# Kernel tuning notes

Measured on AMD Instinct MI355X. Metric: run time of the kernel, lower is better.

The kernel has to match this reference:

```python
import jax, jax.numpy as jnp
import numpy as np

HIDDEN = 2048
NUM_HEADS = 6
HEAD_V = 512          # head_dim * expand_v = 256 * 2
VALUE_DIM = NUM_HEADS * HEAD_V  # 3072
CONV_K = 4
PHASE_BASE = 10000.0
EPS = 1e-5


def _causal_depthwise_conv(x, w):
    # x: [B, T, C], w: [C, K]; causal depthwise conv, no bias, no activation
    B, T, C = x.shape
    K = w.shape[1]
    xp = jnp.pad(x, ((0, 0), (K - 1, 0), (0, 0)))
    y = jnp.zeros_like(x)
    for j in range(K):
        y = y + xp[:, j:j + T, :] * w[:, j]
    return y


def _rotate(x, ang):
    # x: [..., D] interleaved RoPE pairs, ang: [..., D//2] pair angles
    cos = jnp.cos(ang)
    sin = jnp.sin(ang)
    xe = x[..., ::2]
    xo = x[..., 1::2]
    ye = xe * cos - xo * sin
    yo = xo * cos + xe * sin
    return jnp.stack([ye, yo], axis=-1).reshape(x.shape)


def setup_inputs() -> dict:
    key = jax.random.key(0)
    ks = jax.random.split(key, 12)
    s = 0.02
    return {
        "hidden_states": jax.random.normal(ks[0], (2, 2048, HIDDEN), jnp.float32),
        "Wq": jax.random.normal(ks[1], (HIDDEN, VALUE_DIM), jnp.float32) * s,
        "Wk": jax.random.normal(ks[2], (HIDDEN, VALUE_DIM), jnp.float32) * s,
        "Wv": jax.random.normal(ks[3], (HIDDEN, VALUE_DIM), jnp.float32) * s,
        "Wa": jax.random.normal(ks[4], (HIDDEN, NUM_HEADS), jnp.float32) * s,
        "Wb": jax.random.normal(ks[5], (HIDDEN, NUM_HEADS), jnp.float32) * s,
        "Wg": jax.random.normal(ks[6], (HIDDEN, VALUE_DIM), jnp.float32) * s,
        "Wo": jax.random.normal(ks[7], (VALUE_DIM, HIDDEN), jnp.float32) * s,
        "conv_q": jax.random.normal(ks[8], (VALUE_DIM, CONV_K), jnp.float32) * s,
        "conv_k": jax.random.normal(ks[9], (VALUE_DIM, CONV_K), jnp.float32) * s,
        "conv_v": jax.random.normal(ks[10], (VALUE_DIM, CONV_K), jnp.float32) * s,
        "rms_w": jnp.ones((HEAD_V,), jnp.float32),
    }


def _forward(hidden_states, Wq, Wk, Wv, Wa, Wb, Wg, Wo, conv_q, conv_k, conv_v, rms_w):
    B, T, _ = hidden_states.shape
    H, D = NUM_HEADS, HEAD_V
    inv_freq = 1.0 / (PHASE_BASE ** (jnp.arange(0, D, 2, dtype=jnp.float32) / D))  # [D/2]

    q = _causal_depthwise_conv(hidden_states @ Wq, conv_q).reshape(B, T, H, D)
    k = _causal_depthwise_conv(hidden_states @ Wk, conv_k).reshape(B, T, H, D)
    v = _causal_depthwise_conv(hidden_states @ Wv, conv_v).reshape(B, T, H, D)

    # pair angles (RoPE-style): raw even channels scaled by inverse frequencies
    theta = q[..., ::2] * inv_freq           # [B, T, H, D/2] output/query phase
    psi = k[..., ::2] * inv_freq             # write phase
    # state rotation per step = phase increment so cumulative state phase tracks theta
    phi = theta - jnp.concatenate([jnp.zeros_like(theta[:, :1]), theta[:, :-1]], axis=1)

    alpha = jax.nn.sigmoid(hidden_states @ Wa)  # [B, T, H] decay gate
    beta = jax.nn.sigmoid(hidden_states @ Wb)   # [B, T, H] write gate

    # time-major scan inputs
    tm = lambda a: jnp.moveaxis(a, 1, 0)
    xs = (tm(theta), tm(psi), tm(phi), tm(v), tm(alpha), tm(beta))

    def step(state, inp):
        th, ps, ph, vt, at, bt = inp  # state: [B, H, D]
        retained = _rotate(state, ph) * at[..., None]
        write = _rotate(vt, ps)
        new_state = retained + bt[..., None] * write
        out_t = _rotate(new_state, -th)
        return new_state, out_t

    state0 = jnp.zeros((B, H, D), hidden_states.dtype)
    _, out = jax.lax.scan(step, state0, xs)     # out: [T, B, H, D]
    out = jnp.moveaxis(out, 0, 1)               # [B, T, H, D]

    # gated RMSNorm over head_v_dim, then output projection
    g = (hidden_states @ Wg).reshape(B, T, H, D)
    rms = jax.lax.rsqrt(jnp.mean(jnp.square(out), axis=-1, keepdims=True) + EPS)
    o = out * rms * rms_w * jax.nn.silu(g)
    return (o.reshape(B, T, VALUE_DIM) @ Wo)


def reference(hidden_states, Wq, Wk, Wv, Wa, Wb, Wg, Wo, conv_q, conv_k, conv_v, rms_w):
    return _forward(hidden_states, Wq, Wk, Wv, Wa, Wb, Wg, Wo, conv_q, conv_k, conv_v, rms_w)
```

## Files before the change

### kernel.cpp

```cpp
#include <hip/hip_runtime.h>
#include <hip/hip_bf16.h>
#include <stdint.h>

using bf16 = __hip_bfloat16;
using mfrag = __attribute__((ext_vector_type(8))) __bf16;
using f32x4 = __attribute__((ext_vector_type(4))) float;

#define TOKENS 4096
#define HID    2048
#define VD     3072
#define NH     6
#define HD     512
#define NPAIR  256
#define N1     9216
#define NC     64
#define CHUNK  32

__device__ __forceinline__ void gld_lds16(const bf16* g, bf16* l) {
    __builtin_amdgcn_global_load_lds((const __attribute__((address_space(1))) void*)g,
                                     (__attribute__((address_space(3))) void*)l, 16, 0, 0);
}

template<int BN_T>
__global__ __launch_bounds__(512, 2) void k_gemm2(const bf16* __restrict__ A,
                                                  const bf16* __restrict__ Bt,
                                                  void* __restrict__ Cv,
                                                  int M, int N, int K, int obf) {
    constexpr int WN   = (BN_T == 256) ? 4 : 2;
    constexpr int WM   = 8 / WN;
    constexpr int MF   = (256 / WM) / 16;
    constexpr int NHT  = 2 + BN_T / 128;
    constexpr int HT   = 16384;
    constexpr int SLOT = NHT * HT;

    extern __shared__ char smem[];
    const int tid  = threadIdx.x;
    const int wave = tid >> 6;
    const int lane = tid & 63;
    const int lrow = lane & 15;
    const int lk   = lane >> 4;
    const int wm   = wave / WN;
    const int wn   = wave % WN;

    const int nbn = N / BN_T;
    const int bid = blockIdx.x;
    const int xcd = bid & 7;
    const int k   = bid >> 3;
    const int rn  = nbn >> 1;
    const int j   = k & 31;
    const int bm  = ((((xcd >> 1) << 2) + (j & 3)) << 8);
    const int bn  = ((xcd & 1) * rn + (k >> 5) * 8 + (j >> 2)) * BN_T;

    const int NT = K >> 6;

    auto stage_ht = [&](const bf16* src, int row0, char* htb, int koff) {
#pragma unroll
        for (int i = 0; i < 2; ++i) {
            const int L = i * 512 + tid;
            const int r = L >> 3;
            const int c = (L & 7) ^ (r & 7);
            gld_lds16(src + (size_t)(row0 + r) * K + koff + c * 8,
                      (bf16*)(htb + (size_t)L * 16));
        }
    };
    auto STAGE = [&](int t, char* sb) {
        const int ko = t << 6;
        stage_ht(A, bm,       sb,          ko);
        stage_ht(A, bm + 128, sb + HT,     ko);
        stage_ht(Bt, bn,      sb + 2 * HT, ko);
        if (BN_T == 256) stage_ht(Bt, bn + 128, sb + 3 * HT, ko);
    };

    auto rdA = [&](const char* rb, int mf, int kk) -> mfrag {
        const int r  = wm * (MF * 16) + mf * 16 + lrow;
        const int ht = r >> 7, lr = r & 127;
        const int cc = (kk * 4 + lk) ^ (lr & 7);
        return *(const mfrag*)(rb + (size_t)ht * HT + (size_t)lr * 128 + cc * 16);
    };
    auto rdB = [&](const char* rb, int nf, int kk) -> mfrag {
        const int r  = wn * 64 + nf * 16 + lrow;
        const int ht = r >> 7, lr = r & 127;
        const int cc = (kk * 4 + lk) ^ (lr & 7);
        return *(const mfrag*)(rb + (size_t)(2 + ht) * HT + (size_t)lr * 128 + cc * 16);
    };

    f32x4 acc[MF][4];
#pragma unroll
    for (int m = 0; m < MF; ++m)
#pragma unroll
        for (int n = 0; n < 4; ++n) acc[m][n] = f32x4{0.f, 0.f, 0.f, 0.f};

    STAGE(0, smem);
    asm volatile("s_waitcnt vmcnt(0)" ::: "memory");
    __builtin_amdgcn_sched_barrier(0);
    __builtin_amdgcn_s_barrier();

    for (int kt = 0; kt < NT; ++kt) {
        char* rb = smem + (size_t)(kt & 1) * SLOT;
        char* wb = smem + (size_t)((kt + 1) & 1) * SLOT;
        if (kt + 1 < NT) STAGE(kt + 1, wb);

        mfrag bfr[4][2];
#pragma unroll
        for (int nf = 0; nf < 4; ++nf)
#pragma unroll
            for (int kk = 0; kk < 2; ++kk) bfr[nf][kk] = rdB(rb, nf, kk);

#pragma unroll
        for (int h2 = 0; h2 < 2; ++h2) {
            mfrag af[MF / 2][2];
#pragma unroll
            for (int mf = 0; mf < MF / 2; ++mf)
#pragma unroll
                for (int kk = 0; kk < 2; ++kk) af[mf][kk] = rdA(rb, h2 * (MF / 2) + mf, kk);
            __builtin_amdgcn_s_setprio(1);
#pragma unroll
            for (int mf = 0; mf < MF / 2; ++mf)
#pragma unroll
                for (int nf = 0; nf < 4; ++nf) {
                    const int mi = h2 * (MF / 2) + mf;
                    acc[mi][nf] = __builtin_amdgcn_mfma_f32_16x16x32_bf16(af[mf][0], bfr[nf][0], acc[mi][nf], 0, 0, 0);
                    acc[mi][nf] = __builtin_amdgcn_mfma_f32_16x16x32_bf16(af[mf][1], bfr[nf][1], acc[mi][nf], 0, 0, 0);
                }
            __builtin_amdgcn_s_setprio(0);
        }

        if (kt + 1 < NT) {
            asm volatile("s_waitcnt vmcnt(0)" ::: "memory");
            __builtin_amdgcn_sched_barrier(0);
            __builtin_amdgcn_s_barrier();
            __builtin_amdgcn_sched_barrier(0);
        }
    }

#pragma unroll
    for (int m = 0; m < MF; ++m)
#pragma unroll
        for (int j2 = 0; j2 < 4; ++j2) {
            const int r = bm + wm * (MF * 16) + m * 16 + lk * 4 + j2;
#pragma unroll
            for (int n = 0; n < 4; ++n) {
                const int c = bn + wn * 64 + n * 16 + lrow;
                if (obf) ((bf16*)Cv)[(size_t)r * N + c] = __float2bfloat16(acc[m][n][j2]);
                else     ((float*)Cv)[(size_t)r * N + c] = acc[m][n][j2];
            }
        }
}

__global__ void k_prep_w(const float* __restrict__ Wq, const float* __restrict__ Wk,
                         const float* __restrict__ Wv, const float* __restrict__ Wg,
                         bf16* __restrict__ Wt) {
    __shared__ float t[32][33];
    const int n0 = blockIdx.x * 32;
    const int k0 = blockIdx.y * 32;
    const int tx = threadIdx.x, ty = threadIdx.y;
    const float* src; int cb, cs;
    if (n0 < 1536)      { int m = n0;        src = Wq; cb = (m >> 8) * 512 + (m & 255) * 2; cs = 2; }
    else if (n0 < 3072) { int m = n0 - 1536; src = Wk; cb = (m >> 8) * 512 + (m & 255) * 2; cs = 2; }
    else if (n0 < 6144) { int m = n0 - 3072; src = Wv; cb = m; cs = 1; }
    else                { int m = n0 - 6144; src = Wg; cb = m; cs = 1; }
#pragma unroll
    for (int i = 0; i < 4; ++i) {
        int k = k0 + ty + i * 8;
        t[ty + i * 8][tx] = src[(size_t)k * VD + cb + cs * tx];
    }
    __syncthreads();
#pragma unroll
    for (int i = 0; i < 4; ++i) {
        int n = n0 + ty + i * 8;
        Wt[(size_t)n * HID + k0 + tx] = __float2bfloat16(t[tx][ty + i * 8]);
    }
}

__global__ void k_tr_cast(const float* __restrict__ src, bf16* __restrict__ dst, int R, int Ccol) {
    __shared__ float t[32][33];
    const int c0 = blockIdx.x * 32, r0 = blockIdx.y * 32;
    const int tx = threadIdx.x, ty = threadIdx.y;
#pragma unroll
    for (int i = 0; i < 4; ++i)
        t[ty + i * 8][tx] = src[(size_t)(r0 + ty + i * 8) * Ccol + c0 + tx];
    __syncthreads();
#pragma unroll
    for (int i = 0; i < 4; ++i)
        dst[(size_t)(c0 + ty + i * 8) * R + r0 + tx] = __float2bfloat16(t[tx][ty + i * 8]);
}

__global__ __launch_bounds__(256) void k_ab(const float* __restrict__ hs, const float* __restrict__ Wa,
                                            const float* __restrict__ Wb,
                                            float* __restrict__ alpha, float* __restrict__ beta,
                                            bf16* __restrict__ hsb) {
    const int tok = blockIdx.x;
    const int tid = threadIdx.x;
    float part[12];
#pragma unroll
    for (int j = 0; j < 12; ++j) part[j] = 0.f;
    const float* hrow = hs + (size_t)tok * HID;
    bf16* hbrow = hsb + (size_t)tok * HID;
    for (int i = 0; i < 8; ++i) {
        int k = i * 256 + tid;
        float x = hrow[k];
        hbrow[k] = __float2bfloat16(x);
        const float* wa = Wa + k * NH;
        const float* wb = Wb + k * NH;
#pragma unroll
        for (int j = 0; j < NH; ++j) {
            part[j]     = fmaf(x, wa[j], part[j]);
            part[6 + j] = fmaf(x, wb[j], part[6 + j]);
        }
    }
    __shared__ float red[12][4];
    const int lane = tid & 63, wv = tid >> 6;
#pragma unroll
    for (int j = 0; j < 12; ++j) {
        float s = part[j];
        for (int off = 32; off; off >>= 1) s += __shfl_down(s, off);
        if (lane == 0) red[j][wv] = s;
    }
    __syncthreads();
    if (tid < 12) {
        float s = red[tid][0] + red[tid][1] + red[tid][2] + red[tid][3];
        float v = 1.f / (1.f + expf(-s));
        if (tid < 6) alpha[(size_t)tok * NH + tid] = v;
        else         beta [(size_t)tok * NH + tid - 6] = v;
    }
}

__global__ __launch_bounds__(256) void k_scan1(const bf16* __restrict__ X,
                                               const float* __restrict__ alpha,
                                               const float* __restrict__ beta,
                                               const float* __restrict__ cq,
                                               const float* __restrict__ ck,
                                               const float* __restrict__ cv,
                                               float* __restrict__ U, float* __restrict__ pp) {
    const int bx = blockIdx.x;
    const int c  = bx % NC;
    const int h  = (bx / NC) % NH;
    const int b  = bx / (NC * NH);
    const int p  = threadIdx.x;
    const int t0 = c * CHUNK;
    const int ch2 = h * HD + 2 * p;
    const float wq0 = cq[ch2 * 4 + 0], wq1 = cq[ch2 * 4 + 1], wq2 = cq[ch2 * 4 + 2], wq3 = cq[ch2 * 4 + 3];
    const float wk0 = ck[ch2 * 4 + 0], wk1 = ck[ch2 * 4 + 1], wk2 = ck[ch2 * 4 + 2], wk3 = ck[ch2 * 4 + 3];
    const float wa0 = cv[ch2 * 4 + 0], wa1 = cv[ch2 * 4 + 1], wa2 = cv[ch2 * 4 + 2], wa3 = cv[ch2 * 4 + 3];
    const float wb0 = cv[(ch2 + 1) * 4 + 0], wb1 = cv[(ch2 + 1) * 4 + 1],
                wb2 = cv[(ch2 + 1) * 4 + 2], wb3 = cv[(ch2 + 1) * 4 + 3];
    const float invf = exp2f(-13.287712379549449f * ((float)p * (1.0f / 256.0f)));
    const int qcol = h * NPAIR + p;
    const int kcol = 1536 + h * NPAIR + p;
    const int vcol = 3072 + ch2;

    float xq[3], xk[3], xv0[3], xv1[3];
#pragma unroll
    for (int i = 0; i < 3; ++i) {
        int t = t0 - 3 + i;
        if (t >= 0) {
            size_t tok = (size_t)b * 2048 + t;
            const bf16* xr = X + tok * N1;
            xq[i] = __bfloat162float(xr[qcol]);
            xk[i] = __bfloat162float(xr[kcol]);
            __hip_bfloat162 vv = *(const __hip_bfloat162*)&xr[vcol];
            xv0[i] = __bfloat162float(vv.x);
            xv1[i] = __bfloat162float(vv.y);
        } else { xq[i] = xk[i] = xv0[i] = xv1[i] = 0.f; }
    }

    float u0 = 0.f, u1 = 0.f, ap = 1.f;
    for (int t = t0; t < t0 + CHUNK; ++t) {
        const size_t tok = (size_t)b * 2048 + t;
        const bf16* xr = X + tok * N1;
        float nq = __bfloat162float(xr[qcol]);
        float nk = __bfloat162float(xr[kcol]);
        __hip_bfloat162 vv = *(const __hip_bfloat162*)&xr[vcol];
        float nv0 = __bfloat162float(vv.x);
        float nv1 = __bfloat162float(vv.y);
        float yq  = wq3 * nq  + wq2 * xq[2]  + wq1 * xq[1]  + wq0 * xq[0];
        float yk  = wk3 * nk  + wk2 * xk[2]  + wk1 * xk[1]  + wk0 * xk[0];
        float yv0 = wa3 * nv0 + wa2 * xv0[2] + wa1 * xv0[1] + wa0 * xv0[0];
        float yv1 = wb3 * nv1 + wb2 * xv1[2] + wb1 * xv1[1] + wb0 * xv1[0];
        xq[0] = xq[1]; xq[1] = xq[2]; xq[2] = nq;
        xk[0] = xk[1]; xk[1] = xk[2]; xk[2] = nk;
        xv0[0] = xv0[1]; xv0[1] = xv0[2]; xv0[2] = nv0;
        xv1[0] = xv1[1]; xv1[1] = xv1[2]; xv1[2] = nv1;
        float theta = yq * invf, psi = yk * invf;
        float d = psi - theta, sn, cs;
        __sincosf(d, &sn, &cs);
        float w0 = yv0 * cs - yv1 * sn;
        float w1 = yv1 * cs + yv0 * sn;
        float a  = alpha[tok * NH + h];
        float bb = beta [tok * NH + h];
        u0 = fmaf(a, u0, bb * w0);
        u1 = fmaf(a, u1, bb * w1);
        ap *= a;
        *(float2*)&U[tok * (size_t)VD + h * HD + 2 * p] = float2{u0, u1};
        if (p == 0) pp[tok * NH + h] = ap;
    }
}

__global__ __launch_bounds__(512) void k_carry(const float* __restrict__ U, const float* __restrict__ pp,
                                               float* __restrict__ carry) {
    const int bh = blockIdx.x;
    const int b = bh / NH, h = bh % NH;
    const int d = threadIdx.x;
    float ue[NC], pv[NC];
#pragma unroll
    for (int c = 0; c < NC; ++c) {
        size_t tok = (size_t)b * 2048 + c * CHUNK + CHUNK - 1;
        ue[c] = U[tok * (size_t)VD + h * HD + d];
        pv[c] = pp[tok * NH + h];
    }
    float s = 0.f;
#pragma unroll
    for (int c = 0; c < NC; ++c) {
        carry[((size_t)bh * NC + c) * HD + d] = s;
        s = ue[c] + pv[c] * s;
    }
}

__global__ __launch_bounds__(256) void k_pass3(const float* __restrict__ U, const float* __restrict__ pp,
                                               const float* __restrict__ carry, const bf16* __restrict__ X,
                                               const float* __restrict__ rms_w, bf16* __restrict__ O) {
    const int bx = blockIdx.x;
    const int h = bx % NH;
    const size_t tok = bx / NH;
    const int b = (int)(tok >> 11);
    const int t = (int)(tok & 2047);
    const int c = t / CHUNK;
    const int tid = threadIdx.x;
    const int d = tid * 2;
    float2 uu = *(const float2*)&U[tok * (size_t)VD + h * HD + d];
    float  P  = pp[tok * NH + h];
    float2 cy = *(const float2*)&carry[((size_t)(b * NH + h) * NC + c) * HD + d];
    float u0 = fmaf(P, cy.x, uu.x);
    float u1 = fmaf(P, cy.y, uu.y);
    float s = u0 * u0 + u1 * u1;
    for (int off = 32; off; off >>= 1) s += __shfl_down(s, off);
    __shared__ float r4[4];
    const int lane = tid & 63, wv = tid >> 6;
    if (lane == 0) r4[wv] = s;
    __syncthreads();
    float tot = r4[0] + r4[1] + r4[2] + r4[3];
    float rms = rsqrtf(tot * (1.f / 512.f) + 1e-5f);
    __hip_bfloat162 gg = *(const __hip_bfloat162*)&X[tok * N1 + 6144 + h * HD + d];
    float g0 = __bfloat162float(gg.x), g1 = __bfloat162float(gg.y);
    float si0 = g0 / (1.f + expf(-g0));
    float si1 = g1 / (1.f + expf(-g1));
    float o0 = u0 * rms * rms_w[d]     * si0;
    float o1 = u1 * rms * rms_w[d + 1] * si1;
    __hip_bfloat162 ob;
    ob.x = __float2bfloat16(o0);
    ob.y = __float2bfloat16(o1);
    *(__hip_bfloat162*)&O[tok * (size_t)VD + h * HD + d] = ob;
}

extern "C" void kernel_launch(void* const* d_in, const int* in_sizes, int n_in,
                              void* d_out, int out_size, void* d_ws, size_t ws_size,
                              hipStream_t stream) {
    const float* hs   = (const float*)d_in[0];
    const float* Wq   = (const float*)d_in[1];
    const float* Wk   = (const float*)d_in[2];
    const float* Wv   = (const float*)d_in[3];
    const float* Wa   = (const float*)d_in[4];
    const float* Wb   = (const float*)d_in[5];
    const float* Wg   = (const float*)d_in[6];
    const float* Wo   = (const float*)d_in[7];
    const float* cq   = (const float*)d_in[8];
    const float* ck   = (const float*)d_in[9];
    const float* cv   = (const float*)d_in[10];
    const float* rmsw = (const float*)d_in[11];

    char* ws = (char*)d_ws;
    size_t off = 0;
    auto alloc = [&](size_t bytes) -> void* {
        void* p = ws + off;
        off = (off + bytes + 255) & ~(size_t)255;
        return p;
    };
    bf16*  hsb   = (bf16*) alloc((size_t)TOKENS * HID * 2);
    bf16*  Wt    = (bf16*) alloc((size_t)N1 * HID * 2);
    bf16*  Wot   = (bf16*) alloc((size_t)HID * VD * 2);
    bf16*  X     = (bf16*) alloc((size_t)TOKENS * N1 * 2);
    float* U     = (float*)alloc((size_t)TOKENS * VD * 4);
    float* alp   = (float*)alloc((size_t)TOKENS * NH * 4);
    float* bet   = (float*)alloc((size_t)TOKENS * NH * 4);
    float* pp    = (float*)alloc((size_t)TOKENS * NH * 4);
    float* carry = (float*)alloc((size_t)2 * NH * NC * HD * 4);
    bf16*  O     = (bf16*)Wt;

    hipFuncSetAttribute((const void*)k_gemm2<256>,
                        hipFuncAttributeMaxDynamicSharedMemorySize, 2 * 4 * 16384);
    hipFuncSetAttribute((const void*)k_gemm2<128>,
                        hipFuncAttributeMaxDynamicSharedMemorySize, 2 * 3 * 16384);

    k_prep_w<<<dim3(N1 / 32, HID / 32), dim3(32, 8), 0, stream>>>(Wq, Wk, Wv, Wg, Wt);
    k_tr_cast<<<dim3(HID / 32, VD / 32), dim3(32, 8), 0, stream>>>(Wo, Wot, VD, HID);
    k_ab<<<TOKENS, 256, 0, stream>>>(hs, Wa, Wb, alp, bet, hsb);
    k_gemm2<256><<<dim3((TOKENS / 256) * (N1 / 256)), 512, 2 * 4 * 16384, stream>>>(hsb, Wt, X, TOKENS, N1, HID, 1);
    k_scan1<<<2 * NH * NC, 256, 0, stream>>>(X, alp, bet, cq, ck, cv, U, pp);
    k_carry<<<2 * NH, 512, 0, stream>>>(U, pp, carry);
    k_pass3<<<TOKENS * NH, 256, 0, stream>>>(U, pp, carry, X, rmsw, O);
    k_gemm2<128><<<dim3((TOKENS / 256) * (HID / 128)), 512, 2 * 3 * 16384, stream>>>(O, Wot, d_out, TOKENS, HID, VD, 0);
}
```

Baseline: 353.3 us.

## Interleave per-half-tile LDS prefetch with MFMA quarters in GEMM main loop

Restructures the GEMM K-loop into four quarter-phases, each reading a slice of A fragments and issuing one half-tile global-to-LDS stage for the next (or next-next) K step. Prefetch of the B tile runs two steps ahead, and partial vmcnt waits replace the full drain. The aim is to spread memory issue across the compute and hide load latency better. In exchange it adds a barrier per quarter and tighter buffer reuse, which risks sync overhead or races on the double buffer.

```diff
diff --git a/kernel.cpp b/kernel.cpp
--- a/kernel.cpp
+++ b/kernel.cpp
@@ -22,13 +22,14 @@
 }
 
 template<int BN_T>
-__global__ __launch_bounds__(512, 2) void k_gemm2(const bf16* __restrict__ A,
+__global__ __launch_bounds__(512, 2) void k_gemm3(const bf16* __restrict__ A,
                                                   const bf16* __restrict__ Bt,
                                                   void* __restrict__ Cv,
                                                   int M, int N, int K, int obf) {
     constexpr int WN   = (BN_T == 256) ? 4 : 2;
     constexpr int WM   = 8 / WN;
     constexpr int MF   = (256 / WM) / 16;
+    constexpr int AQ   = MF / 4;
     constexpr int NHT  = 2 + BN_T / 128;
     constexpr int HT   = 16384;
     constexpr int SLOT = NHT * HT;
@@ -63,12 +64,14 @@
                       (bf16*)(htb + (size_t)L * 16));
         }
     };
-    auto STAGE = [&](int t, char* sb) {
+    auto ST = [&](int which, int t) {
+        if (t >= NT) return;
+        char* sb = smem + (size_t)(t & 1) * SLOT;
         const int ko = t << 6;
-        stage_ht(A, bm,       sb,          ko);
-        stage_ht(A, bm + 128, sb + HT,     ko);
-        stage_ht(Bt, bn,      sb + 2 * HT, ko);
-        if (BN_T == 256) stage_ht(Bt, bn + 128, sb + 3 * HT, ko);
+        if      (which == 0) stage_ht(A,  bm,       sb + 0 * HT, ko);
+        else if (which == 1) stage_ht(A,  bm + 128, sb + 1 * HT, ko);
+        else if (which == 2) stage_ht(Bt, bn,       sb + 2 * HT, ko);
+        else                 stage_ht(Bt, bn + 128, sb + 3 * HT, ko);
     };
 
     auto rdA = [&](const char* rb, int mf, int kk) -> mfrag {
@@ -90,46 +93,62 @@
 #pragma unroll
         for (int n = 0; n < 4; ++n) acc[m][n] = f32x4{0.f, 0.f, 0.f, 0.f};
 
-    STAGE(0, smem);
-    asm volatile("s_waitcnt vmcnt(0)" ::: "memory");
+    ST(2, 0);
+    if (BN_T == 256) ST(3, 0);
+    ST(0, 0);
+    ST(1, 0);
+    ST(2, 1);
+    asm volatile("s_waitcnt vmcnt(2)" ::: "memory");
     __builtin_amdgcn_sched_barrier(0);
     __builtin_amdgcn_s_barrier();
 
     for (int kt = 0; kt < NT; ++kt) {
-        char* rb = smem + (size_t)(kt & 1) * SLOT;
-        char* wb = smem + (size_t)((kt + 1) & 1) * SLOT;
-        if (kt + 1 < NT) STAGE(kt + 1, wb);
-
+        const char* rb = smem + (size_t)(kt & 1) * SLOT;
         mfrag bfr[4][2];
 #pragma unroll
-        for (int nf = 0; nf < 4; ++nf)
-#pragma unroll
-            for (int kk = 0; kk < 2; ++kk) bfr[nf][kk] = rdB(rb, nf, kk);
-
-#pragma unroll
-        for (int h2 = 0; h2 < 2; ++h2) {
-            mfrag af[MF / 2][2];
-#pragma unroll
-            for (int mf = 0; mf < MF / 2; ++mf)
-#pragma unroll
-                for (int kk = 0; kk < 2; ++kk) af[mf][kk] = rdA(rb, h2 * (MF / 2) + mf, kk);
+        for (int q = 0; q < 4; ++q) {
+            if (q == 0) {
+#pragma unroll
+                for (int nf = 0; nf < 4; ++nf)
+#pragma unroll
+                    for (int kk = 0; kk < 2; ++kk) bfr[nf][kk] = rdB(rb, nf, kk);
+            }
+            mfrag af[AQ][2];
+#pragma unroll
+            for (int i = 0; i < AQ; ++i)
+#pragma unroll
+                for (int kk = 0; kk < 2; ++kk) af[i][kk] = rdA(rb, q * AQ + i, kk);
+
+            if (BN_T == 256) {
+                if      (q == 0) ST(3, kt + 1);
+                else if (q == 1) ST(0, kt + 1);
+                else if (q == 2) ST(1, kt + 1);
+                else             ST(2, kt + 2);
+            } else {
+                if      (q == 0) ST(0, kt + 1);
+                else if (q == 1) ST(1, kt + 1);
+                else if (q == 2) ST(2, kt + 2);
+            }
+            if (q == 3 && kt + 1 < NT) {
+                if (kt + 2 < NT) { asm volatile("s_waitcnt vmcnt(2)" ::: "memory"); }
+                else             { asm volatile("s_waitcnt vmcnt(0)" ::: "memory"); }
+            }
+            __builtin_amdgcn_sched_barrier(0);
+            __builtin_amdgcn_s_barrier();
+            asm volatile("s_waitcnt lgkmcnt(0)" ::: "memory");
+            __builtin_amdgcn_sched_barrier(0);
             __builtin_amdgcn_s_setprio(1);
 #pragma unroll
-            for (int mf = 0; mf < MF / 2; ++mf)
+            for (int i = 0; i < AQ; ++i)
 #pragma unroll
                 for (int nf = 0; nf < 4; ++nf) {
-                    const int mi = h2 * (MF / 2) + mf;
-                    acc[mi][nf] = __builtin_amdgcn_mfma_f32_16x16x32_bf16(af[mf][0], bfr[nf][0], acc[mi][nf], 0, 0, 0);
-                    acc[mi][nf] = __builtin_amdgcn_mfma_f32_16x16x32_bf16(af[mf][1], bfr[nf][1], acc[mi][nf], 0, 0, 0);
+                    const int mi = q * AQ + i;
+                    acc[mi][nf] = __builtin_amdgcn_mfma_f32_16x16x32_bf16(af[i][0], bfr[nf][0], acc[mi][nf], 0, 0, 0);
+                    acc[mi][nf] = __builtin_amdgcn_mfma_f32_16x16x32_bf16(af[i][1], bfr[nf][1], acc[mi][nf], 0, 0, 0);
                 }
             __builtin_amdgcn_s_setprio(0);
-        }
-
-        if (kt + 1 < NT) {
-            asm volatile("s_waitcnt vmcnt(0)" ::: "memory");
             __builtin_amdgcn_sched_barrier(0);
             __builtin_amdgcn_s_barrier();
-            __builtin_amdgcn_sched_barrier(0);
         }
     }
 
@@ -386,17 +405,17 @@
     float* carry = (float*)alloc((size_t)2 * NH * NC * HD * 4);
     bf16*  O     = (bf16*)Wt;
 
-    hipFuncSetAttribute((const void*)k_gemm2<256>,
+    hipFuncSetAttribute((const void*)k_gemm3<256>,
                         hipFuncAttributeMaxDynamicSharedMemorySize, 2 * 4 * 16384);
-    hipFuncSetAttribute((const void*)k_gemm2<128>,
+    hipFuncSetAttribute((const void*)k_gemm3<128>,
                         hipFuncAttributeMaxDynamicSharedMemorySize, 2 * 3 * 16384);
 
     k_prep_w<<<dim3(N1 / 32, HID / 32), dim3(32, 8), 0, stream>>>(Wq, Wk, Wv, Wg, Wt);
     k_tr_cast<<<dim3(HID / 32, VD / 32), dim3(32, 8), 0, stream>>>(Wo, Wot, VD, HID);
     k_ab<<<TOKENS, 256, 0, stream>>>(hs, Wa, Wb, alp, bet, hsb);
-    k_gemm2<256><<<dim3((TOKENS / 256) * (N1 / 256)), 512, 2 * 4 * 16384, stream>>>(hsb, Wt, X, TOKENS, N1, HID, 1);
+    k_gemm3<256><<<dim3((TOKENS / 256) * (N1 / 256)), 512, 2 * 4 * 16384, stream>>>(hsb, Wt, X, TOKENS, N1, HID, 1);
     k_scan1<<<2 * NH * NC, 256, 0, stream>>>(X, alp, bet, cq, ck, cv, U, pp);
     k_carry<<<2 * NH, 512, 0, stream>>>(U, pp, carry);
     k_pass3<<<TOKENS * NH, 256, 0, stream>>>(U, pp, carry, X, rmsw, O);
-    k_gemm2<128><<<dim3((TOKENS / 256) * (HID / 128)), 512, 2 * 3 * 16384, stream>>>(O, Wot, d_out, TOKENS, HID, VD, 0);
-}
+    k_gemm3<128><<<dim3((TOKENS / 256) * (HID / 128)), 512, 2 * 3 * 16384, stream>>>(O, Wot, d_out, TOKENS, HID, VD, 0);
+}
```

New measurement: 369.8 us. +4.7%, slower.

## Split GEMM k-tile staging into four phases interleaved with MFMA quarters

Applied to the files above, without the earlier changes.

The GEMM main loop now splits each k-tile's compute into four MFMA phases. The next tile's global-to-LDS loads are issued in pieces (B halves and A row units) between those phases, and each phase is gated by a partial vmcnt wait plus a barrier instead of one full drain per tile. A-tile staging is reorganised so each unit loads exactly the rows a given MFMA quarter consumes. The goal is to overlap memory traffic with matrix math and avoid the stall at the end of every tile, at the cost of more barriers per iteration and fragile hand-tuned wait counts.

```diff
diff --git a/kernel.cpp b/kernel.cpp
--- a/kernel.cpp
+++ b/kernel.cpp
@@ -21,14 +21,20 @@
                                      (__attribute__((address_space(3))) void*)l, 16, 0, 0);
 }
 
+#define VMWAIT(n) asm volatile("s_waitcnt vmcnt(" #n ")" ::: "memory")
+#define SCHED0    __builtin_amdgcn_sched_barrier(0)
+#define SBAR      __builtin_amdgcn_s_barrier()
+
 template<int BN_T>
-__global__ __launch_bounds__(512, 2) void k_gemm2(const bf16* __restrict__ A,
+__global__ __launch_bounds__(512, 2) void k_gemm4(const bf16* __restrict__ A,
                                                   const bf16* __restrict__ Bt,
                                                   void* __restrict__ Cv,
                                                   int M, int N, int K, int obf) {
     constexpr int WN   = (BN_T == 256) ? 4 : 2;
     constexpr int WM   = 8 / WN;
     constexpr int MF   = (256 / WM) / 16;
+    constexpr int AQ   = MF / 4;
+    constexpr int SH   = AQ * 16;
     constexpr int NHT  = 2 + BN_T / 128;
     constexpr int HT   = 16384;
     constexpr int SLOT = NHT * HT;
@@ -45,30 +51,38 @@
     const int nbn = N / BN_T;
     const int bid = blockIdx.x;
     const int xcd = bid & 7;
-    const int k   = bid >> 3;
+    const int kk2 = bid >> 3;
     const int rn  = nbn >> 1;
-    const int j   = k & 31;
-    const int bm  = ((((xcd >> 1) << 2) + (j & 3)) << 8);
-    const int bn  = ((xcd & 1) * rn + (k >> 5) * 8 + (j >> 2)) * BN_T;
+    const int jj  = kk2 & 31;
+    const int bm  = ((((xcd >> 1) << 2) + (jj & 3)) << 8);
+    const int bn  = ((xcd & 1) * rn + (kk2 >> 5) * 8 + (jj >> 2)) * BN_T;
 
     const int NT = K >> 6;
 
-    auto stage_ht = [&](const bf16* src, int row0, char* htb, int koff) {
+    auto ST_B = [&](int half, int t) {
+        char* sb = smem + (size_t)(t & 1) * SLOT + (2 + half) * HT;
+        const int ko = t << 6;
 #pragma unroll
         for (int i = 0; i < 2; ++i) {
             const int L = i * 512 + tid;
             const int r = L >> 3;
             const int c = (L & 7) ^ (r & 7);
-            gld_lds16(src + (size_t)(row0 + r) * K + koff + c * 8,
-                      (bf16*)(htb + (size_t)L * 16));
+            gld_lds16(Bt + (size_t)(bn + half * 128 + r) * K + ko + c * 8,
+                      (bf16*)(sb + (size_t)L * 16));
         }
     };
-    auto STAGE = [&](int t, char* sb) {
+    auto ST_A = [&](int unit, int t) {
+        char* sb = smem + (size_t)(t & 1) * SLOT;
         const int ko = t << 6;
-        stage_ht(A, bm,       sb,          ko);
-        stage_ht(A, bm + 128, sb + HT,     ko);
-        stage_ht(Bt, bn,      sb + 2 * HT, ko);
-        if (BN_T == 256) stage_ht(Bt, bn + 128, sb + 3 * HT, ko);
+        const int s  = tid / (SH * 8);
+        const int W  = tid % (SH * 8);
+        const int rl = W >> 3;
+        const int c  = W & 7;
+        const int r256 = s * (256 / WM) + unit * SH + rl;
+        const int cl = c ^ (r256 & 7);
+        const int ht = r256 >> 7, lr = r256 & 127;
+        gld_lds16(A + (size_t)(bm + r256) * K + ko + cl * 8,
+                  (bf16*)(sb + (size_t)ht * HT + (size_t)lr * 128 + c * 16));
     };
 
     auto rdA = [&](const char* rb, int mf, int kk) -> mfrag {
@@ -90,48 +104,66 @@
 #pragma unroll
         for (int n = 0; n < 4; ++n) acc[m][n] = f32x4{0.f, 0.f, 0.f, 0.f};
 
-    STAGE(0, smem);
-    asm volatile("s_waitcnt vmcnt(0)" ::: "memory");
-    __builtin_amdgcn_sched_barrier(0);
-    __builtin_amdgcn_s_barrier();
+    ST_B(0, 0);
+    if (BN_T == 256) ST_B(1, 0);
+    ST_A(0, 0); ST_A(1, 0); ST_A(2, 0); ST_A(3, 0);
+
+#define MFMA_PHASE(q)                                                              \
+    {                                                                              \
+        mfrag af[AQ][2];                                                           \
+        _Pragma("unroll")                                                          \
+        for (int i = 0; i < AQ; ++i)                                               \
+            _Pragma("unroll")                                                      \
+            for (int kx = 0; kx < 2; ++kx) af[i][kx] = rdA(rb, (q) * AQ + i, kx);  \
+        SCHED0;                                                                    \
+        __builtin_amdgcn_s_setprio(1);                                             \
+        _Pragma("unroll")                                                          \
+        for (int i = 0; i < AQ; ++i)                                               \
+            _Pragma("unroll")                                                      \
+            for (int nf = 0; nf < 4; ++nf) {                                       \
+                const int mi = (q) * AQ + i;                                       \
+                acc[mi][nf] = __builtin_amdgcn_mfma_f32_16x16x32_bf16(af[i][0], bfr[nf][0], acc[mi][nf], 0, 0, 0); \
+                acc[mi][nf] = __builtin_amdgcn_mfma_f32_16x16x32_bf16(af[i][1], bfr[nf][1], acc[mi][nf], 0, 0, 0); \
+            }                                                                      \
+        __builtin_amdgcn_s_setprio(0);                                             \
+    }
 
     for (int kt = 0; kt < NT; ++kt) {
-        char* rb = smem + (size_t)(kt & 1) * SLOT;
-        char* wb = smem + (size_t)((kt + 1) & 1) * SLOT;
-        if (kt + 1 < NT) STAGE(kt + 1, wb);
-
+        const char* rb = smem + (size_t)(kt & 1) * SLOT;
+        const bool last = (kt == NT - 1);
         mfrag bfr[4][2];
+
+        VMWAIT(3);
+        SCHED0; SBAR;
 #pragma unroll
         for (int nf = 0; nf < 4; ++nf)
 #pragma unroll
-            for (int kk = 0; kk < 2; ++kk) bfr[nf][kk] = rdB(rb, nf, kk);
-
-#pragma unroll
-        for (int h2 = 0; h2 < 2; ++h2) {
-            mfrag af[MF / 2][2];
-#pragma unroll
-            for (int mf = 0; mf < MF / 2; ++mf)
-#pragma unroll
-                for (int kk = 0; kk < 2; ++kk) af[mf][kk] = rdA(rb, h2 * (MF / 2) + mf, kk);
-            __builtin_amdgcn_s_setprio(1);
-#pragma unroll
-            for (int mf = 0; mf < MF / 2; ++mf)
-#pragma unroll
-                for (int nf = 0; nf < 4; ++nf) {
-                    const int mi = h2 * (MF / 2) + mf;
-                    acc[mi][nf] = __builtin_amdgcn_mfma_f32_16x16x32_bf16(af[mf][0], bfr[nf][0], acc[mi][nf], 0, 0, 0);
-                    acc[mi][nf] = __builtin_amdgcn_mfma_f32_16x16x32_bf16(af[mf][1], bfr[nf][1], acc[mi][nf], 0, 0, 0);
-                }
-            __builtin_amdgcn_s_setprio(0);
+            for (int kx = 0; kx < 2; ++kx) bfr[nf][kx] = rdB(rb, nf, kx);
+        if (!last) ST_B(0, kt + 1);
+        MFMA_PHASE(0)
+
+        if (last) { VMWAIT(2); } else { VMWAIT(4); }
+        SCHED0; SBAR;
+        if (!last) {
+            if (BN_T == 256) ST_B(1, kt + 1);
+            else             { ST_A(0, kt + 1); ST_A(1, kt + 1); }
         }
-
-        if (kt + 1 < NT) {
-            asm volatile("s_waitcnt vmcnt(0)" ::: "memory");
-            __builtin_amdgcn_sched_barrier(0);
-            __builtin_amdgcn_s_barrier();
-            __builtin_amdgcn_sched_barrier(0);
+        MFMA_PHASE(1)
+
+        if (last) { VMWAIT(1); } else { VMWAIT(5); }
+        SCHED0; SBAR;
+        if (!last) {
+            if (BN_T == 256) { ST_A(0, kt + 1); ST_A(1, kt + 1); }
+            else             { ST_A(2, kt + 1); ST_A(3, kt + 1); }
         }
-    }
+        MFMA_PHASE(2)
+
+        if (last) { VMWAIT(0); } else { VMWAIT(6); }
+        SCHED0; SBAR;
+        if (!last && BN_T == 256) { ST_A(2, kt + 1); ST_A(3, kt + 1); }
+        MFMA_PHASE(3)
+    }
+#undef MFMA_PHASE
 
 #pragma unroll
     for (int m = 0; m < MF; ++m)
@@ -386,17 +418,17 @@
     float* carry = (float*)alloc((size_t)2 * NH * NC * HD * 4);
     bf16*  O     = (bf16*)Wt;
 
-    hipFuncSetAttribute((const void*)k_gemm2<256>,
+    hipFuncSetAttribute((const void*)k_gemm4<256>,
                         hipFuncAttributeMaxDynamicSharedMemorySize, 2 * 4 * 16384);
-    hipFuncSetAttribute((const void*)k_gemm2<128>,
+    hipFuncSetAttribute((const void*)k_gemm4<128>,
                         hipFuncAttributeMaxDynamicSharedMemorySize, 2 * 3 * 16384);
 
     k_prep_w<<<dim3(N1 / 32, HID / 32), dim3(32, 8), 0, stream>>>(Wq, Wk, Wv, Wg, Wt);
     k_tr_cast<<<dim3(HID / 32, VD / 32), dim3(32, 8), 0, stream>>>(Wo, Wot, VD, HID);
     k_ab<<<TOKENS, 256, 0, stream>>>(hs, Wa, Wb, alp, bet, hsb);
-    k_gemm2<256><<<dim3((TOKENS / 256) * (N1 / 256)), 512, 2 * 4 * 16384, stream>>>(hsb, Wt, X, TOKENS, N1, HID, 1);
+    k_gemm4<256><<<dim3((TOKENS / 256) * (N1 / 256)), 512, 2 * 4 * 16384, stream>>>(hsb, Wt, X, TOKENS, N1, HID, 1);
     k_scan1<<<2 * NH * NC, 256, 0, stream>>>(X, alp, bet, cq, ck, cv, U, pp);
     k_carry<<<2 * NH, 512, 0, stream>>>(U, pp, carry);
     k_pass3<<<TOKENS * NH, 256, 0, stream>>>(U, pp, carry, X, rmsw, O);
-    k_gemm2<128><<<dim3((TOKENS / 256) * (HID / 128)), 512, 2 * 3 * 16384, stream>>>(O, Wot, d_out, TOKENS, HID, VD, 0);
-}
+    k_gemm4<128><<<dim3((TOKENS / 256) * (HID / 128)), 512, 2 * 3 * 16384, stream>>>(O, Wot, d_out, TOKENS, HID, VD, 0);
+}
```

Result: no change. 347.7 us (-1.6%).
